# Kernel optimization log

Measured on AMD Instinct MI355X. Metric: run time of the kernel, lower is better.

The kernel has to match this reference:

```python
import jax, jax.numpy as jnp
import numpy as np

D = 768    # text_feature_dim (BERT)
H = 1024   # hidden_dim
L = 16384  # history length


def setup_inputs() -> dict:
    key = jax.random.key(0)
    ks = jax.random.split(key, 10)
    text_v = jax.random.normal(ks[0], (1, D), dtype=jnp.float32)
    result = jax.random.uniform(ks[1], (1,), dtype=jnp.float32)
    text_s = jax.random.normal(ks[2], (L, D), dtype=jnp.float32)
    hidden_s = jax.random.normal(ks[3], (L, H), dtype=jnp.float32)
    # GRU params (PyTorch layout: W_ih [3H, 2D], W_hh [3H, H]), uniform(-1/sqrt(H), 1/sqrt(H))
    s = 1.0 / np.sqrt(H)
    W_ih = jax.random.uniform(ks[4], (3 * H, 2 * D), minval=-s, maxval=s, dtype=jnp.float32)
    W_hh = jax.random.uniform(ks[5], (3 * H, H), minval=-s, maxval=s, dtype=jnp.float32)
    b_ih = jax.random.uniform(ks[6], (3 * H,), minval=-s, maxval=s, dtype=jnp.float32)
    b_hh = jax.random.uniform(ks[7], (3 * H,), minval=-s, maxval=s, dtype=jnp.float32)
    # score layer: Linear(D+H, 1)
    s2 = 1.0 / np.sqrt(D + H)
    score_W = jax.random.uniform(ks[8], (1, D + H), minval=-s2, maxval=s2, dtype=jnp.float32)
    score_b = jax.random.uniform(ks[9], (1,), minval=-s2, maxval=s2, dtype=jnp.float32)
    return {"text_v": text_v, "result": result, "text_s": text_s, "hidden_s": hidden_s,
            "W_ih": W_ih, "W_hh": W_hh, "b_ih": b_ih, "b_hh": b_hh,
            "score_W": score_W, "score_b": score_b}


def reference(text_v, result, text_s, hidden_s, W_ih, W_hh, b_ih, b_hh, score_W, score_b):
    # --- attention over growing history ---
    h = hidden_s[-1:, :]                                   # [1, H] last hidden state
    alpha = jax.nn.softmax(text_s @ text_v.T, axis=0)      # [L, 1]
    attn_h = alpha.T @ hidden_s                            # [1, H]

    # --- score prediction ---
    pred_v = jnp.concatenate([text_v, attn_h], axis=1)     # [1, D+H]
    score = pred_v @ score_W.T + score_b                   # [1, 1]

    # --- input gating by correctness ---
    zeros = jnp.zeros_like(text_v)
    x_r = jnp.where(result >= 0.5,
                    jnp.concatenate([text_v, zeros], axis=1),
                    jnp.concatenate([zeros, text_v], axis=1))  # [1, 2D]

    # --- GRU cell (PyTorch gate order: r, z, n) ---
    gi = x_r @ W_ih.T + b_ih                               # [1, 3H]
    gh = h @ W_hh.T + b_hh                                 # [1, 3H]
    i_r, i_z, i_n = jnp.split(gi, 3, axis=1)
    h_r, h_z, h_n = jnp.split(gh, 3, axis=1)
    r = jax.nn.sigmoid(i_r + h_r)
    z = jax.nn.sigmoid(i_z + h_z)
    n = jnp.tanh(i_n + r * h_n)
    h_new = (1.0 - z) * n + z * h                          # [1, H]

    return score[0], h_new                                 # score.squeeze(0) -> [1]
```

## Files before the change

### kernel.cpp

```cpp
#include <hip/hip_runtime.h>
#include <math.h>

#define LL 16384
#define Dm 768
#define Hm 1024

#define ATT_B 1024
#define GI_B  192
#define GH_B  192
#define MID_B 32

#define WS_GI 0
#define WS_GH 3072
#define WS_PM 6144
#define WS_PS 7168
#define WS_PV 8192
#define WS_M2 (8192 + 1024*1024)
#define WS_S2 (WS_M2 + 32)
#define WS_V2 (WS_S2 + 32)

__device__ __forceinline__ float dot4(float4 a, float4 b) {
    return a.x*b.x + a.y*b.y + a.z*b.z + a.w*b.w;
}

__global__ __launch_bounds__(256) void k_main(
    const float* __restrict__ text_v, const float* __restrict__ result,
    const float* __restrict__ text_s, const float* __restrict__ hidden_s,
    const float* __restrict__ W_ih, const float* __restrict__ W_hh,
    const float* __restrict__ b_ih, const float* __restrict__ b_hh,
    float* __restrict__ ws)
{
    const int b    = blockIdx.x;
    const int tid  = threadIdx.x;
    const int lane = tid & 63;
    const int wv   = tid >> 6;

    if (b < ATT_B) {
        __shared__ float dots[16];
        __shared__ float wts[16];
        const int row0  = b * 16;
        const int rbase = wv * 4;

        float4 tv0 = *(const float4*)(text_v + 4*lane);
        float4 tv1 = *(const float4*)(text_v + 4*lane + 256);
        float4 tv2 = *(const float4*)(text_v + 4*lane + 512);

        float4 x[4][3];
        #pragma unroll
        for (int i = 0; i < 4; ++i) {
            const float* p = text_s + (size_t)(row0 + rbase + i)*Dm + 4*lane;
            x[i][0] = *(const float4*)(p);
            x[i][1] = *(const float4*)(p + 256);
            x[i][2] = *(const float4*)(p + 512);
        }
        #pragma unroll
        for (int i = 0; i < 4; ++i) {
            float s = dot4(x[i][0], tv0) + dot4(x[i][1], tv1) + dot4(x[i][2], tv2);
            #pragma unroll
            for (int o = 32; o; o >>= 1) s += __shfl_xor(s, o);
            if (lane == 0) dots[rbase + i] = s;
        }

        float4 hv[2][8];
        #pragma unroll
        for (int r = 0; r < 8; ++r)
            hv[0][r] = *(const float4*)(hidden_s + (size_t)(row0 + r)*Hm + 4*tid);

        __syncthreads();
        float m = dots[0];
        #pragma unroll
        for (int r = 1; r < 16; ++r) m = fmaxf(m, dots[r]);
        if (tid < 16) wts[tid] = expf(dots[tid] - m);
        __syncthreads();

        float4 acc = {0.f, 0.f, 0.f, 0.f};
        #pragma unroll
        for (int c = 0; c < 2; ++c) {
            if (c < 1) {
                #pragma unroll
                for (int r = 0; r < 8; ++r)
                    hv[1][r] = *(const float4*)(hidden_s + (size_t)(row0 + 8 + r)*Hm + 4*tid);
            }
            #pragma unroll
            for (int r = 0; r < 8; ++r) {
                const float w = wts[c*8 + r];
                acc.x += w*hv[c][r].x; acc.y += w*hv[c][r].y;
                acc.z += w*hv[c][r].z; acc.w += w*hv[c][r].w;
            }
        }
        *(float4*)(ws + WS_PV + (size_t)b*1024 + 4*tid) = acc;
        if (tid == 0) {
            float s = 0.f;
            #pragma unroll
            for (int r = 0; r < 16; ++r) s += wts[r];
            ws[WS_PM + b] = m;
            ws[WS_PS + b] = s;
        }
    } else if (b < ATT_B + GI_B) {
        const int gb  = b - ATT_B;
        const int off = (result[0] >= 0.5f) ? 0 : Dm;
        float4 tv0 = *(const float4*)(text_v + 4*lane);
        float4 tv1 = *(const float4*)(text_v + 4*lane + 256);
        float4 tv2 = *(const float4*)(text_v + 4*lane + 512);
        const int kbase = gb*16 + wv*4;
        float4 x[4][3];
        #pragma unroll
        for (int i = 0; i < 4; ++i) {
            const float* p = W_ih + (size_t)(kbase + i)*(2*Dm) + off + 4*lane;
            x[i][0] = *(const float4*)(p);
            x[i][1] = *(const float4*)(p + 256);
            x[i][2] = *(const float4*)(p + 512);
        }
        #pragma unroll
        for (int i = 0; i < 4; ++i) {
            float s = dot4(x[i][0], tv0) + dot4(x[i][1], tv1) + dot4(x[i][2], tv2);
            #pragma unroll
            for (int o = 32; o; o >>= 1) s += __shfl_xor(s, o);
            const int k = kbase + i;
            if (lane == 0) ws[WS_GI + k] = s + b_ih[k];
        }
    } else {
        const int hb = b - ATT_B - GI_B;
        const float* h = hidden_s + (size_t)(LL - 1)*Hm;
        float4 h0 = *(const float4*)(h + 4*lane);
        float4 h1 = *(const float4*)(h + 4*lane + 256);
        float4 h2 = *(const float4*)(h + 4*lane + 512);
        float4 h3 = *(const float4*)(h + 4*lane + 768);
        const int kbase = hb*16 + wv*4;
        float4 x[4][4];
        #pragma unroll
        for (int i = 0; i < 4; ++i) {
            const float* p = W_hh + (size_t)(kbase + i)*Hm + 4*lane;
            x[i][0] = *(const float4*)(p);
            x[i][1] = *(const float4*)(p + 256);
            x[i][2] = *(const float4*)(p + 512);
            x[i][3] = *(const float4*)(p + 768);
        }
        #pragma unroll
        for (int i = 0; i < 4; ++i) {
            float s = dot4(x[i][0], h0) + dot4(x[i][1], h1)
                    + dot4(x[i][2], h2) + dot4(x[i][3], h3);
            #pragma unroll
            for (int o = 32; o; o >>= 1) s += __shfl_xor(s, o);
            const int k = kbase + i;
            if (lane == 0) ws[WS_GH + k] = s + b_hh[k];
        }
    }
}

__global__ __launch_bounds__(256) void k_mid(float* __restrict__ ws) {
    __shared__ float sm[32];
    __shared__ float sc[32];
    const int b  = blockIdx.x;
    const int t  = threadIdx.x;
    const int p0 = b * 32;
    if (t < 32) sm[t] = ws[WS_PM + p0 + t];
    __syncthreads();
    float m = sm[0];
    #pragma unroll
    for (int r = 1; r < 32; ++r) m = fmaxf(m, sm[r]);
    if (t < 32) sc[t] = expf(sm[t] - m);
    __syncthreads();

    float4 acc = {0.f, 0.f, 0.f, 0.f};
    float4 hv[2][8];
    #pragma unroll
    for (int r = 0; r < 8; ++r)
        hv[0][r] = *(const float4*)(ws + WS_PV + (size_t)(p0 + r)*1024 + 4*t);
    #pragma unroll
    for (int c = 0; c < 4; ++c) {
        if (c < 3) {
            #pragma unroll
            for (int r = 0; r < 8; ++r)
                hv[(c+1)&1][r] = *(const float4*)(ws + WS_PV + (size_t)(p0 + (c+1)*8 + r)*1024 + 4*t);
        }
        #pragma unroll
        for (int r = 0; r < 8; ++r) {
            const float w = sc[c*8 + r];
            acc.x += w*hv[c&1][r].x; acc.y += w*hv[c&1][r].y;
            acc.z += w*hv[c&1][r].z; acc.w += w*hv[c&1][r].w;
        }
    }
    *(float4*)(ws + WS_V2 + (size_t)b*1024 + 4*t) = acc;
    if (t == 0) {
        float s = 0.f;
        #pragma unroll
        for (int r = 0; r < 32; ++r) s += sc[r] * ws[WS_PS + p0 + r];
        ws[WS_M2 + b] = m;
        ws[WS_S2 + b] = s;
    }
}

__global__ __launch_bounds__(1024) void k_final(
    const float* __restrict__ text_v, const float* __restrict__ hidden_s,
    const float* __restrict__ score_W, const float* __restrict__ score_b,
    float* __restrict__ ws, float* __restrict__ out)
{
    __shared__ float sred[16];
    const int tid = threadIdx.x;
    float M = ws[WS_M2];
    #pragma unroll
    for (int r = 1; r < 32; ++r) M = fmaxf(M, ws[WS_M2 + r]);
    float S = 0.f, a = 0.f;
    #pragma unroll
    for (int r = 0; r < 32; ++r) {
        const float scl = expf(ws[WS_M2 + r] - M);
        S += scl * ws[WS_S2 + r];
        a += scl * ws[WS_V2 + r*1024 + tid];
    }
    a /= S;
    float sp = a * score_W[Dm + tid];
    if (tid < Dm) sp += text_v[tid] * score_W[tid];
    #pragma unroll
    for (int o = 32; o; o >>= 1) sp += __shfl_xor(sp, o);
    if ((tid & 63) == 0) sred[tid >> 6] = sp;
    __syncthreads();
    if (tid == 0) {
        float s = score_b[0];
        #pragma unroll
        for (int i = 0; i < 16; ++i) s += sred[i];
        out[0] = s;
    }
    const float gi_r = ws[WS_GI + tid];
    const float gi_z = ws[WS_GI + 1024 + tid];
    const float gi_n = ws[WS_GI + 2048 + tid];
    const float gh_r = ws[WS_GH + tid];
    const float gh_z = ws[WS_GH + 1024 + tid];
    const float gh_n = ws[WS_GH + 2048 + tid];
    const float hprev = hidden_s[(size_t)(LL - 1)*Hm + tid];
    const float r = 1.f / (1.f + expf(-(gi_r + gh_r)));
    const float z = 1.f / (1.f + expf(-(gi_z + gh_z)));
    const float n = tanhf(gi_n + r*gh_n);
    out[1 + tid] = (1.f - z)*n + z*hprev;
}

extern "C" void kernel_launch(void* const* d_in, const int* in_sizes, int n_in,
                              void* d_out, int out_size, void* d_ws, size_t ws_size,
                              hipStream_t stream) {
    const float* text_v   = (const float*)d_in[0];
    const float* result   = (const float*)d_in[1];
    const float* text_s   = (const float*)d_in[2];
    const float* hidden_s = (const float*)d_in[3];
    const float* W_ih     = (const float*)d_in[4];
    const float* W_hh     = (const float*)d_in[5];
    const float* b_ih     = (const float*)d_in[6];
    const float* b_hh     = (const float*)d_in[7];
    const float* score_W  = (const float*)d_in[8];
    const float* score_b  = (const float*)d_in[9];
    float* out = (float*)d_out;
    float* ws  = (float*)d_ws;

    k_main <<<ATT_B + GI_B + GH_B, 256, 0, stream>>>(
        text_v, result, text_s, hidden_s, W_ih, W_hh, b_ih, b_hh, ws);
    k_mid  <<<MID_B, 256, 0, stream>>>(ws);
    k_final<<<1, 1024, 0, stream>>>(text_v, hidden_s, score_W, score_b, ws, out);
}
```

Measured before the change: 187.5 us.

## Compute per-wavefront attention partials over 8 rows to drop block syncs

The attention blocks now give each wavefront its own 8-row chunk. Each wavefront computes the dot products, softmax max and sum, and weighted hidden-state accumulation entirely in registers, with no shared memory or __syncthreads. This halves the attention block count and doubles the number of partial results (2048 partials of 1024 floats). The mid and final reduction kernels are resized to 64 groups, and the final kernel batches loads in chunks of 8. In exchange the kernel writes and reads back twice as much partial-vector workspace, and per-thread register use is higher.

After: 193.6 us. +3.2%, slower.

```diff
diff --git a/kernel.cpp b/kernel.cpp
--- a/kernel.cpp
+++ b/kernel.cpp
@@ -5,19 +5,20 @@
 #define Dm 768
 #define Hm 1024
 
-#define ATT_B 1024
+#define ATT_B 512
 #define GI_B  192
 #define GH_B  192
-#define MID_B 32
+#define NP    2048
+#define MID_B 64
 
 #define WS_GI 0
 #define WS_GH 3072
 #define WS_PM 6144
-#define WS_PS 7168
-#define WS_PV 8192
-#define WS_M2 (8192 + 1024*1024)
-#define WS_S2 (WS_M2 + 32)
-#define WS_V2 (WS_S2 + 32)
+#define WS_PS 8192
+#define WS_PV 10240
+#define WS_M2 (10240 + 2048*1024)
+#define WS_S2 (WS_M2 + 64)
+#define WS_V2 (WS_S2 + 64)
 
 __device__ __forceinline__ float dot4(float4 a, float4 b) {
     return a.x*b.x + a.y*b.y + a.z*b.z + a.w*b.w;
@@ -36,65 +37,64 @@
     const int wv   = tid >> 6;
 
     if (b < ATT_B) {
-        __shared__ float dots[16];
-        __shared__ float wts[16];
-        const int row0  = b * 16;
-        const int rbase = wv * 4;
+        const int wid = b*4 + wv;
+        const int r0  = wid*8;
 
         float4 tv0 = *(const float4*)(text_v + 4*lane);
         float4 tv1 = *(const float4*)(text_v + 4*lane + 256);
         float4 tv2 = *(const float4*)(text_v + 4*lane + 512);
 
-        float4 x[4][3];
-        #pragma unroll
-        for (int i = 0; i < 4; ++i) {
-            const float* p = text_s + (size_t)(row0 + rbase + i)*Dm + 4*lane;
+        float4 x[8][3];
+        #pragma unroll
+        for (int i = 0; i < 8; ++i) {
+            const float* p = text_s + (size_t)(r0 + i)*Dm + 4*lane;
             x[i][0] = *(const float4*)(p);
             x[i][1] = *(const float4*)(p + 256);
             x[i][2] = *(const float4*)(p + 512);
         }
-        #pragma unroll
-        for (int i = 0; i < 4; ++i) {
-            float s = dot4(x[i][0], tv0) + dot4(x[i][1], tv1) + dot4(x[i][2], tv2);
-            #pragma unroll
-            for (int o = 32; o; o >>= 1) s += __shfl_xor(s, o);
-            if (lane == 0) dots[rbase + i] = s;
-        }
-
-        float4 hv[2][8];
-        #pragma unroll
-        for (int r = 0; r < 8; ++r)
-            hv[0][r] = *(const float4*)(hidden_s + (size_t)(row0 + r)*Hm + 4*tid);
-
-        __syncthreads();
-        float m = dots[0];
-        #pragma unroll
-        for (int r = 1; r < 16; ++r) m = fmaxf(m, dots[r]);
-        if (tid < 16) wts[tid] = expf(dots[tid] - m);
-        __syncthreads();
-
-        float4 acc = {0.f, 0.f, 0.f, 0.f};
+        float pd[8];
+        #pragma unroll
+        for (int i = 0; i < 8; ++i)
+            pd[i] = dot4(x[i][0], tv0) + dot4(x[i][1], tv1) + dot4(x[i][2], tv2);
+        #pragma unroll
+        for (int i = 0; i < 8; ++i) {
+            #pragma unroll
+            for (int o = 32; o; o >>= 1) pd[i] += __shfl_xor(pd[i], o);
+        }
+
+        float m = pd[0];
+        #pragma unroll
+        for (int i = 1; i < 8; ++i) m = fmaxf(m, pd[i]);
+        float w[8], s = 0.f;
+        #pragma unroll
+        for (int i = 0; i < 8; ++i) { w[i] = expf(pd[i] - m); s += w[i]; }
+
+        float4 acc[4] = {{0,0,0,0},{0,0,0,0},{0,0,0,0},{0,0,0,0}};
         #pragma unroll
         for (int c = 0; c < 2; ++c) {
-            if (c < 1) {
+            float4 hv[4][4];
+            #pragma unroll
+            for (int j = 0; j < 4; ++j) {
+                const float* p = hidden_s + (size_t)(r0 + c*4 + j)*Hm + 4*lane;
                 #pragma unroll
-                for (int r = 0; r < 8; ++r)
-                    hv[1][r] = *(const float4*)(hidden_s + (size_t)(row0 + 8 + r)*Hm + 4*tid);
+                for (int k = 0; k < 4; ++k) hv[j][k] = *(const float4*)(p + 256*k);
             }
             #pragma unroll
-            for (int r = 0; r < 8; ++r) {
-                const float w = wts[c*8 + r];
-                acc.x += w*hv[c][r].x; acc.y += w*hv[c][r].y;
-                acc.z += w*hv[c][r].z; acc.w += w*hv[c][r].w;
+            for (int j = 0; j < 4; ++j) {
+                const float wj = w[c*4 + j];
+                #pragma unroll
+                for (int k = 0; k < 4; ++k) {
+                    acc[k].x += wj*hv[j][k].x; acc[k].y += wj*hv[j][k].y;
+                    acc[k].z += wj*hv[j][k].z; acc[k].w += wj*hv[j][k].w;
+                }
             }
         }
-        *(float4*)(ws + WS_PV + (size_t)b*1024 + 4*tid) = acc;
-        if (tid == 0) {
-            float s = 0.f;
-            #pragma unroll
-            for (int r = 0; r < 16; ++r) s += wts[r];
-            ws[WS_PM + b] = m;
-            ws[WS_PS + b] = s;
+        #pragma unroll
+        for (int k = 0; k < 4; ++k)
+            *(float4*)(ws + WS_PV + (size_t)wid*1024 + 4*lane + 256*k) = acc[k];
+        if (lane == 0) {
+            ws[WS_PM + wid] = m;
+            ws[WS_PS + wid] = s;
         }
     } else if (b < ATT_B + GI_B) {
         const int gb  = b - ATT_B;
@@ -163,22 +163,17 @@
     __syncthreads();
 
     float4 acc = {0.f, 0.f, 0.f, 0.f};
-    float4 hv[2][8];
-    #pragma unroll
-    for (int r = 0; r < 8; ++r)
-        hv[0][r] = *(const float4*)(ws + WS_PV + (size_t)(p0 + r)*1024 + 4*t);
     #pragma unroll
     for (int c = 0; c < 4; ++c) {
-        if (c < 3) {
-            #pragma unroll
-            for (int r = 0; r < 8; ++r)
-                hv[(c+1)&1][r] = *(const float4*)(ws + WS_PV + (size_t)(p0 + (c+1)*8 + r)*1024 + 4*t);
-        }
+        float4 hv[8];
+        #pragma unroll
+        for (int r = 0; r < 8; ++r)
+            hv[r] = *(const float4*)(ws + WS_PV + (size_t)(p0 + c*8 + r)*1024 + 4*t);
         #pragma unroll
         for (int r = 0; r < 8; ++r) {
             const float w = sc[c*8 + r];
-            acc.x += w*hv[c&1][r].x; acc.y += w*hv[c&1][r].y;
-            acc.z += w*hv[c&1][r].z; acc.w += w*hv[c&1][r].w;
+            acc.x += w*hv[r].x; acc.y += w*hv[r].y;
+            acc.z += w*hv[r].z; acc.w += w*hv[r].w;
         }
     }
     *(float4*)(ws + WS_V2 + (size_t)b*1024 + 4*t) = acc;
@@ -198,15 +193,27 @@
 {
     __shared__ float sred[16];
     const int tid = threadIdx.x;
-    float M = ws[WS_M2];
-    #pragma unroll
-    for (int r = 1; r < 32; ++r) M = fmaxf(M, ws[WS_M2 + r]);
+    float mbuf[8], M;
+    #pragma unroll
+    for (int i = 0; i < 8; ++i) mbuf[i] = ws[WS_M2 + i*8];
+    M = ws[WS_M2];
+    #pragma unroll
+    for (int r = 1; r < 64; ++r) M = fmaxf(M, ws[WS_M2 + r]);
+    (void)mbuf;
     float S = 0.f, a = 0.f;
     #pragma unroll
-    for (int r = 0; r < 32; ++r) {
-        const float scl = expf(ws[WS_M2 + r] - M);
-        S += scl * ws[WS_S2 + r];
-        a += scl * ws[WS_V2 + r*1024 + tid];
+    for (int c = 0; c < 8; ++c) {
+        float scl[8], vv[8];
+        #pragma unroll
+        for (int r = 0; r < 8; ++r) {
+            scl[r] = expf(ws[WS_M2 + c*8 + r] - M);
+            vv[r]  = ws[WS_V2 + (c*8 + r)*1024 + tid];
+        }
+        #pragma unroll
+        for (int r = 0; r < 8; ++r) {
+            S += scl[r] * ws[WS_S2 + c*8 + r];
+            a += scl[r] * vv[r];
+        }
     }
     a /= S;
     float sp = a * score_W[Dm + tid];
```
